# Kernel tuning notes

Hardware: AMD Instinct MI355X
Metric: run time of the kernel (lower is better)

## Reference

```python
import jax, jax.numpy as jnp
import numpy as np

B, D = 8192, 512
MARGIN, CR_BETA, NUM_CLASSES = 0.2, 0.1, 1000


def setup_inputs() -> dict:
    key = jax.random.key(0)
    k1, k2, k3, k4 = jax.random.split(key, 4)
    return {
        "img": jax.random.normal(k1, (B, D), jnp.float32),
        "txt": jax.random.normal(k2, (B, D), jnp.float32),
        "txt_cr": jax.random.normal(k3, (B, D), jnp.float32),
        "labels": jax.random.randint(k4, (B,), 0, NUM_CLASSES),
        "auto_margin_flag": 1,
        "margin": jnp.full((B,), MARGIN, jnp.float32),  # opt.margin repeated per row
        "cr_beta": CR_BETA,
    }


def _similarity(a, b):
    # row-normalize then full cosine-similarity matrix + matched (diagonal) sims
    an = a / (jnp.linalg.norm(a, axis=1, keepdims=True) + 1e-8)
    bn = b / (jnp.linalg.norm(b, axis=1, keepdims=True) + 1e-8)
    return an @ bn.T, jnp.sum(an * bn, axis=1)


def _dir_loss(sim, labels, margin, auto_flag):
    # semi-hard negative mining per anchor row, fully vectorized.
    # Deterministic stand-in for np.random.choice: first valid negative index.
    diag = jnp.diagonal(sim)                               # sim[idx, idx]
    neg_mask = labels[None, :] != labels[:, None]          # [B,B] negatives
    loss_mat = sim - diag[:, None] + margin[:, None]       # triplet margin term
    valid = neg_mask & (loss_mat > 0) & (loss_mat < margin[:, None])
    valid = jax.lax.stop_gradient(valid)                   # mining is detached (numpy in torch)
    has_valid = jnp.any(valid, axis=1)
    if auto_flag:
        row_ok = (margin >= 0.16) & has_valid
    else:
        row_ok = has_valid
    neg_idx = jnp.argmax(valid, axis=1)                    # first valid negative
    sim_an = jnp.take_along_axis(sim, neg_idx[:, None], axis=1)[:, 0]
    per_row = jax.nn.relu(margin - diag + sim_an)
    return jnp.sum(jnp.where(row_ok, per_row, 0.0))


def _cr_loss(img, txt, txt_cr, labels, auto_flag, margin, cr_beta):
    sim, sm = _similarity(img, txt)
    sim_cr, sm_cr = _similarity(img, txt_cr)
    if auto_flag:
        lam = jnp.abs(jax.lax.stop_gradient(sm_cr)) / jnp.abs(jax.lax.stop_gradient(sm))
        lam = jnp.minimum(lam, 1.0)                        # clamp lambda_cr to <= 1
        margin_cr = (lam + 1.0) * margin / 2.0
    else:
        margin_cr = margin / 2.0
    margin_cr = jax.lax.stop_gradient(margin_cr)
    base = _dir_loss(sim, labels, margin, auto_flag) + _dir_loss(sim.T, labels, margin, auto_flag)
    cr = _dir_loss(sim_cr, labels, margin_cr, auto_flag) + _dir_loss(sim_cr.T, labels, margin_cr, auto_flag)
    return base + cr_beta * cr


def reference(img, txt, txt_cr, labels, auto_margin_flag, margin, cr_beta):
    return _cr_loss(img, txt, txt_cr, labels, bool(auto_margin_flag), margin, cr_beta)
```

## Files before the change

kernel.cpp:

```cpp
#include <hip/hip_runtime.h>
#include <climits>

#define NB 8192
#define ND 512
#define NSPLIT 32
#define RSTART 64
#define RSPAN ((NB - RSTART + NSPLIT - 1) / NSPLIT)


__global__ __launch_bounds__(256) void stats_k(
        const float* __restrict__ img, const float* __restrict__ txt,
        const float* __restrict__ cr, const float* __restrict__ margin,
        const int* __restrict__ flagp,
        float* rnImg, float* rnTxt, float* rnCr,
        float* dgSim, float* dgCr, float* mgCr,
        int* negIdx, int* stragCnt, float* out) {
    int tid = threadIdx.x, bid = blockIdx.x;
    int g = bid * 256 + tid;
    if (g < 4 * NB) negIdx[g] = INT_MAX;
    if (bid == 0 && tid < 8) stragCnt[tid] = 0;
    if (bid == 0 && tid == 0) out[0] = 0.0f;

    int r = bid * 16 + (tid >> 4);
    int q = tid & 15;
    const float4* iv = (const float4*)(img + (size_t)r * ND);
    const float4* tv = (const float4*)(txt + (size_t)r * ND);
    const float4* cv = (const float4*)(cr  + (size_t)r * ND);
    float sii = 0, stt = 0, scc = 0, sit = 0, sic = 0;
    #pragma unroll
    for (int i = 0; i < 8; ++i) {
        int k = q + i * 16;
        float4 x = iv[k], y = tv[k], w = cv[k];
        sii += x.x*x.x + x.y*x.y + x.z*x.z + x.w*x.w;
        stt += y.x*y.x + y.y*y.y + y.z*y.z + y.w*y.w;
        scc += w.x*w.x + w.y*w.y + w.z*w.z + w.w*w.w;
        sit += x.x*y.x + x.y*y.y + x.z*y.z + x.w*y.w;
        sic += x.x*w.x + x.y*w.y + x.z*w.z + x.w*w.w;
    }
    #pragma unroll
    for (int off = 1; off < 16; off <<= 1) {
        sii += __shfl_xor(sii, off); stt += __shfl_xor(stt, off);
        scc += __shfl_xor(scc, off); sit += __shfl_xor(sit, off);
        sic += __shfl_xor(sic, off);
    }
    if (q == 0) {
        float rnI = 1.0f / (sqrtf(sii) + 1e-8f);
        float rnT = 1.0f / (sqrtf(stt) + 1e-8f);
        float rnC = 1.0f / (sqrtf(scc) + 1e-8f);
        float ds = sit * rnI * rnT;
        float dc = sic * rnI * rnC;
        float m  = margin[r];
        float mcr = flagp[0] ? (fminf(fabsf(dc) / fabsf(ds), 1.0f) + 1.0f) * m * 0.5f
                             : m * 0.5f;
        rnImg[r] = rnI; rnTxt[r] = rnT; rnCr[r] = rnC;
        dgSim[r] = ds;  dgCr[r]  = dc;  mgCr[r] = mcr;
    }
}

__device__ inline void pass_arrays(int z,
        const float* img, const float* txt, const float* cr,
        const float* rnImg, const float* rnTxt, const float* rnCr,
        const float* dgSim, const float* dgCr,
        const float* margin, const float* mgCr,
        const float*& A, const float*& B, const float*& rnA, const float*& rnB,
        const float*& dgA, const float*& mgA) {
    if (z == 0)      { A = img; B = txt; rnA = rnImg; rnB = rnTxt; dgA = dgSim; mgA = margin; }
    else if (z == 1) { A = txt; B = img; rnA = rnTxt; rnB = rnImg; dgA = dgSim; mgA = margin; }
    else if (z == 2) { A = img; B = cr;  rnA = rnImg; rnB = rnCr;  dgA = dgCr;  mgA = mgCr;   }
    else             { A = cr;  B = img; rnA = rnCr;  rnB = rnImg; dgA = dgCr;  mgA = mgCr;   }
}

__global__ __launch_bounds__(256) void band_k(
        const float* __restrict__ img, const float* __restrict__ txt,
        const float* __restrict__ cr, const int* __restrict__ labels,
        const int* __restrict__ flagp, const float* __restrict__ margin,
        const float* __restrict__ betap,
        const float* rnImg, const float* rnTxt, const float* rnCr,
        const float* dgSim, const float* dgCr, const float* mgCr,
        int* stragCnt, int* stragList, float* out) {
    __shared__ __align__(16) float As[16][64];
    __shared__ __align__(16) float Bs[16][64];
    __shared__ float aRn[64], aDg[64], aMg[64], colRn[64];
    __shared__ int   aLab[64], colLab[64], resIdx[64];
    __shared__ float blockAcc;

    const int tid = threadIdx.x, z = blockIdx.y, a0 = blockIdx.x * 64;
    const int flag = flagp[0];
    const float *A, *B, *rnA, *rnB, *dgA, *mgA;
    pass_arrays(z, img, txt, cr, rnImg, rnTxt, rnCr, dgSim, dgCr, margin, mgCr,
                A, B, rnA, rnB, dgA, mgA);

    if (tid < 64) {
        int a = a0 + tid;
        float mg = mgA[a];
        aRn[tid] = rnA[a]; aDg[tid] = dgA[a]; aMg[tid] = mg;
        aLab[tid] = labels[a];
        colRn[tid] = rnB[tid]; colLab[tid] = labels[tid];
        resIdx[tid] = (flag && mg < 0.16f) ? -1 : INT_MAX;
    }
    if (tid == 0) blockAcc = 0.0f;

    const int ty4  = (tid >> 4) * 4, tx4 = (tid & 15) * 4;
    const int lrow = tid >> 2,  lk4 = (tid & 3) * 4;

    float acc[4][4];
    #pragma unroll
    for (int i = 0; i < 4; ++i)
        #pragma unroll
        for (int j = 0; j < 4; ++j) acc[i][j] = 0.0f;

    float4 va = *(const float4*)(A + (size_t)(a0 + lrow) * ND + lk4);
    float4 vb = *(const float4*)(B + (size_t)lrow * ND + lk4);
    for (int kc = 0; kc < ND; kc += 16) {
        __syncthreads();
        As[lk4 + 0][lrow] = va.x; As[lk4 + 1][lrow] = va.y;
        As[lk4 + 2][lrow] = va.z; As[lk4 + 3][lrow] = va.w;
        Bs[lk4 + 0][lrow] = vb.x; Bs[lk4 + 1][lrow] = vb.y;
        Bs[lk4 + 2][lrow] = vb.z; Bs[lk4 + 3][lrow] = vb.w;
        if (kc + 16 < ND) {
            va = *(const float4*)(A + (size_t)(a0 + lrow) * ND + kc + 16 + lk4);
            vb = *(const float4*)(B + (size_t)lrow * ND + kc + 16 + lk4);
        }
        __syncthreads();
        #pragma unroll
        for (int k = 0; k < 16; ++k) {
            float4 av = *(const float4*)&As[k][ty4];
            float4 bv = *(const float4*)&Bs[k][tx4];
            float ar[4] = {av.x, av.y, av.z, av.w};
            float br[4] = {bv.x, bv.y, bv.z, bv.w};
            #pragma unroll
            for (int i = 0; i < 4; ++i)
                #pragma unroll
                for (int j = 0; j < 4; ++j)
                    acc[i][j] = fmaf(ar[i], br[j], acc[i][j]);
        }
    }
    __syncthreads();

    #pragma unroll
    for (int i = 0; i < 4; ++i) {
        int r = ty4 + i;
        float mgv = aMg[r];
        if (flag && mgv < 0.16f) continue;
        float dg = aDg[r], rna = aRn[r];
        int la = aLab[r];
        #pragma unroll
        for (int j = 0; j < 4; ++j) {
            int c = tx4 + j;
            if (colLab[c] == la) continue;
            float v  = acc[i][j] * rna * colRn[c];
            float lm = v - dg + mgv;
            if (lm > 0.0f && lm < mgv) atomicMin(&resIdx[r], c);
        }
    }
    __syncthreads();

    #pragma unroll
    for (int i = 0; i < 4; ++i) {
        int r = ty4 + i;
        int w = resIdx[r];
        if (w < 0 || w == INT_MAX) continue;
        int c = w - tx4;
        if (c < 0 || c > 3) continue;
        float v  = acc[i][c] * aRn[r] * colRn[w];
        float lm = v - aDg[r] + aMg[r];
        atomicAdd(&blockAcc, lm);
    }
    __syncthreads();

    if (tid < 64 && resIdx[tid] == INT_MAX) {
        int pos = atomicAdd(&stragCnt[z], 1);
        stragList[z * NB + pos] = a0 + tid;
    }
    if (tid == 0 && blockAcc != 0.0f) {
        float scale = (z >= 2) ? betap[0] : 1.0f;
        atomicAdd(out, blockAcc * scale);
    }
}

__device__ inline float dot8(const float4& a0, const float4& a1,
                             const float4& b0, const float4& b1) {
    return a0.x*b0.x + a0.y*b0.y + a0.z*b0.z + a0.w*b0.w
         + a1.x*b1.x + a1.y*b1.y + a1.z*b1.z + a1.w*b1.w;
}

__global__ __launch_bounds__(256) void strag_k(
        const float* __restrict__ img, const float* __restrict__ txt,
        const float* __restrict__ cr, const int* __restrict__ labels,
        const float* rnImg, const float* rnTxt, const float* rnCr,
        const float* dgSim, const float* dgCr,
        const float* __restrict__ margin, const float* mgCr,
        const int* stragCnt, const int* stragList, int* negIdx) {
    __shared__ float colDot[64];
    __shared__ int   cMin;
    __shared__ int   sharedG;
    const int tid = threadIdx.x;
    const int wv = tid >> 6, lane = tid & 63;

    const int s0c = stragCnt[0], s1c = stragCnt[1];
    const int s2c = stragCnt[2], s3c = stragCnt[3];
    const int ST = s0c + s1c + s2c + s3c;
    const int total = ST * NSPLIT;

    for (int it = blockIdx.x; it < total; it += gridDim.x) {
        int rg = it / ST;
        int sIdx = it - rg * ST;
        int z, s;
        if (sIdx < s0c)                 { z = 0; s = sIdx; }
        else if ((sIdx -= s0c) < s1c)   { z = 1; s = sIdx; }
        else if ((sIdx -= s1c) < s2c)   { z = 2; s = sIdx; }
        else                            { z = 3; s = sIdx - s2c; }
        const float *A, *B, *rnA, *rnB, *dgA, *mgA;
        pass_arrays(z, img, txt, cr, rnImg, rnTxt, rnCr, dgSim, dgCr,
                    margin, mgCr, A, B, rnA, rnB, dgA, mgA);
        int a = stragList[z * NB + s];
        int* gp = &negIdx[z * NB + a];
        const int start = RSTART + rg * RSPAN;
        const int rEnd = min(start + RSPAN, NB);

        __syncthreads();
        if (tid == 0) { cMin = INT_MAX; sharedG = atomicMin(gp, INT_MAX); }
        __syncthreads();
        int end = min(rEnd, sharedG);
        if (start >= end) continue;

        float rna = rnA[a], dgv = dgA[a], mgv = mgA[a];
        int la = labels[a];
        const float4* Av = (const float4*)(A + (size_t)a * ND);
        float4 ar0 = Av[lane], ar1 = Av[lane + 64];

        for (int j0 = start; j0 < end; j0 += 64) {
            #pragma unroll
            for (int g = 0; g < 2; ++g) {
                int cbase = j0 + wv * 16 + g * 8;
                float4 b0[8], b1[8];
                #pragma unroll
                for (int q = 0; q < 8; ++q) {
                    int col = cbase + q;
                    const float4* Bv = (col < end)
                        ? (const float4*)(B + (size_t)col * ND)
                        : (const float4*)B;
                    b0[q] = Bv[lane]; b1[q] = Bv[lane + 64];
                }
                float d[8];
                #pragma unroll
                for (int q = 0; q < 8; ++q) d[q] = dot8(ar0, ar1, b0[q], b1[q]);
                #pragma unroll
                for (int off = 1; off < 64; off <<= 1) {
                    #pragma unroll
                    for (int q = 0; q < 8; ++q) d[q] += __shfl_xor(d[q], off);
                }
                if (lane == 0) {
                    #pragma unroll
                    for (int q = 0; q < 8; ++q)
                        colDot[wv * 16 + g * 8 + q] = d[q];
                }
            }
            __syncthreads();
            if (tid < 64) {
                int col = j0 + tid;
                if (col < end && labels[col] != la) {
                    float lm = colDot[tid] * rna * rnB[col] - dgv + mgv;
                    if (lm > 0.0f && lm < mgv) atomicMin(&cMin, col);
                }
            } else if (tid == 64) {
                sharedG = atomicMin(gp, INT_MAX);
            }
            __syncthreads();
            int found = cMin;
            int gmin  = sharedG;
            if (found != INT_MAX) {
                if (tid == 0) atomicMin(gp, found);
                break;
            }
            if (gmin <= start) break;
            if (gmin < end) end = gmin;
        }
    }
}

__global__ __launch_bounds__(256) void final_k(
        const float* __restrict__ img, const float* __restrict__ txt,
        const float* __restrict__ cr,
        const float* rnImg, const float* rnTxt, const float* rnCr,
        const float* dgSim, const float* dgCr,
        const float* __restrict__ margin, const float* mgCr,
        const float* __restrict__ betap,
        const int* stragCnt, const int* stragList, const int* negIdx,
        float* out) {
    __shared__ float s4[4];
    const int tid = threadIdx.x, z = blockIdx.y;
    const float *A, *B, *rnA, *rnB, *dgA, *mgA;
    pass_arrays(z, img, txt, cr, rnImg, rnTxt, rnCr, dgSim, dgCr, margin, mgCr,
                A, B, rnA, rnB, dgA, mgA);
    int t = blockIdx.x * 256 + tid;
    float contrib = 0.0f;
    if (t < stragCnt[z]) {
        int a = stragList[z * NB + t];
        int idx = negIdx[z * NB + a];
        if (idx != INT_MAX) {
            const float4* Av = (const float4*)(A + (size_t)a   * ND);
            const float4* Bv = (const float4*)(B + (size_t)idx * ND);
            float d = 0.0f;
            #pragma unroll 8
            for (int i = 0; i < ND / 4; ++i) {
                float4 x = Av[i], y = Bv[i];
                d += x.x*y.x + x.y*y.y + x.z*y.z + x.w*y.w;
            }
            float lm = d * rnA[a] * rnB[idx] - dgA[a] + mgA[a];
            contrib = fmaxf(lm, 0.0f);
        }
    }
    #pragma unroll
    for (int off = 32; off; off >>= 1) contrib += __shfl_xor(contrib, off);
    if ((tid & 63) == 0) s4[tid >> 6] = contrib;
    __syncthreads();
    if (tid == 0) {
        float sum = s4[0] + s4[1] + s4[2] + s4[3];
        if (sum != 0.0f) atomicAdd(out, sum * ((z >= 2) ? betap[0] : 1.0f));
    }
}


__global__ __launch_bounds__(256) void zero_k(float* out, int n) {
    int g = blockIdx.x * 256 + threadIdx.x;
    if (g < n) out[g] = 0.0f;
}

template <int U>
__device__ void stragScan(const float* __restrict__ A, const float* __restrict__ B,
                          const int* __restrict__ labels, int a0, int u, int scol,
                          const int* sList, int g0,
                          const float* aRn, const float* aDg, const float* aMg,
                          const int* aLab, int* sMin8, int* doneMask,
                          float* blockAcc) {
    const int tid = threadIdx.x;
    float rn_s[U], dg_s[U], mg_s[U];
    int lab_s[U];
    const float4* Av[U];
    #pragma unroll
    for (int s = 0; s < U; ++s) {
        int slot = sList[g0 + (s < u ? s : 0)];
        rn_s[s] = aRn[slot]; dg_s[s] = aDg[slot]; mg_s[s] = aMg[slot];
        lab_s[s] = aLab[slot];
        Av[s] = (const float4*)(A + (size_t)(a0 + slot) * ND);
    }
    if (tid < U) sMin8[tid] = INT_MAX;
    if (tid == 0) *doneMask = 0;
    __syncthreads();
    for (int jb = scol; jb < NB; jb += 256) {
        int j = jb + tid;
        bool jv = (j < NB);
        int mask = *doneMask;
        float dot[U];
        #pragma unroll
        for (int s = 0; s < U; ++s) dot[s] = 0.0f;
        float ssq = 0.0f;
        if (jv) {
            const float4* Bv = (const float4*)(B + (size_t)j * ND);
            #pragma unroll 4
            for (int k4 = 0; k4 < ND / 4; ++k4) {
                float4 b = Bv[k4];
                ssq += b.x*b.x + b.y*b.y + b.z*b.z + b.w*b.w;
                #pragma unroll
                for (int s = 0; s < U; ++s) {
                    float4 a = Av[s][k4];
                    dot[s] += a.x*b.x + a.y*b.y + a.z*b.z + a.w*b.w;
                }
            }
        }
        float rnb = 1.0f / (sqrtf(ssq) + 1e-8f);
        int lj = jv ? labels[j] : -1;
        float lmv[U];
        #pragma unroll
        for (int s = 0; s < U; ++s) {
            lmv[s] = dot[s] * rn_s[s] * rnb - dg_s[s] + mg_s[s];
            if (jv && s < u && !((mask >> s) & 1) && lj != lab_s[s] &&
                lmv[s] > 0.0f && lmv[s] < mg_s[s])
                atomicMin(&sMin8[s], j);
        }
        __syncthreads();
        #pragma unroll
        for (int s = 0; s < U; ++s)
            if (jv && s < u && !((mask >> s) & 1) && sMin8[s] == j)
                atomicAdd(blockAcc, lmv[s]);
        __syncthreads();
        if (tid == 0) {
            int m2 = 0;
            for (int s = 0; s < u; ++s)
                if (sMin8[s] != INT_MAX) m2 |= (1 << s);
            *doneMask = m2;
        }
        __syncthreads();
        if (*doneMask == (1 << u) - 1) break;
    }
}

__global__ __launch_bounds__(256) void mine_k(const float* __restrict__ img,
                                              const float* __restrict__ txt,
                                              const float* __restrict__ cr,
                                              const int*   __restrict__ labels,
                                              const int*   __restrict__ flagp,
                                              const float* __restrict__ margin,
                                              const float* __restrict__ betap,
                                              float* __restrict__ out) {
    __shared__ __align__(16) float As[16][64];
    __shared__ __align__(16) float Bs[16][64];
    __shared__ float aRn[64], aDg[64], aMg[64];
    __shared__ int   aLab[64];
    __shared__ float colRn[64];
    __shared__ int   colLab[64];
    __shared__ int   resIdx[64], prevIdx[64];
    __shared__ int   cnt;
    __shared__ float blockAcc;
    __shared__ int   sList[64];
    __shared__ int   sCnt;
    __shared__ int   sMin8[8];
    __shared__ int   doneMask;

    const int tid  = threadIdx.x;
    const int z    = blockIdx.y;
    const int a0   = blockIdx.x * 64;
    const int flag = flagp[0];
    const float* A = (z == 1) ? txt : (z == 3) ? cr : img;
    const float* B = (z == 0) ? txt : (z == 2) ? cr : img;
    {
        int ar = tid >> 2, q = tid & 3;
        int a  = a0 + ar;
        const float4* iv = (const float4*)(img + (size_t)a * ND) + q * 32;
        const float4* tv = (const float4*)(txt + (size_t)a * ND) + q * 32;
        const float4* cv = (const float4*)(cr  + (size_t)a * ND) + q * 32;
        float sii = 0, stt = 0, scc = 0, sit = 0, sic = 0;
        #pragma unroll 4
        for (int i = 0; i < 32; ++i) {
            float4 x = iv[i], y = tv[i], w = cv[i];
            sii += x.x*x.x + x.y*x.y + x.z*x.z + x.w*x.w;
            stt += y.x*y.x + y.y*y.y + y.z*y.z + y.w*y.w;
            scc += w.x*w.x + w.y*w.y + w.z*w.z + w.w*w.w;
            sit += x.x*y.x + x.y*y.y + x.z*y.z + x.w*y.w;
            sic += x.x*w.x + x.y*w.y + x.z*w.z + x.w*w.w;
        }
        sii += __shfl_xor(sii, 1); sii += __shfl_xor(sii, 2);
        stt += __shfl_xor(stt, 1); stt += __shfl_xor(stt, 2);
        sit += __shfl_xor(sit, 1); sit += __shfl_xor(sit, 2);
        scc += __shfl_xor(scc, 1); scc += __shfl_xor(scc, 2);
        sic += __shfl_xor(sic, 1); sic += __shfl_xor(sic, 2);
        if (q == 0) {
            float rnI = 1.0f / (sqrtf(sii) + 1e-8f);
            float rnT = 1.0f / (sqrtf(stt) + 1e-8f);
            float ds  = sit * rnI * rnT;
            float m   = margin[a];
            float mg, rna, dgv;
            if (z >= 2) {
                float rnC = 1.0f / (sqrtf(scc) + 1e-8f);
                float dc  = sic * rnI * rnC;
                mg = flag ? (fminf(fabsf(dc) / fabsf(ds), 1.0f) + 1.0f) * m * 0.5f
                          : m * 0.5f;
                dgv = dc; rna = (z == 3) ? rnC : rnI;
            } else {
                mg = m; dgv = ds; rna = (z == 1) ? rnT : rnI;
            }
            aRn[ar] = rna; aDg[ar] = dgv; aMg[ar] = mg; aLab[ar] = labels[a];
            resIdx[ar] = (flag && mg < 0.16f) ? -1 : INT_MAX;
        }
        if (tid == 0) blockAcc = 0.0f;
    }
    __syncthreads();
    const int ty4  = (tid >> 4) * 4, tx4 = (tid & 15) * 4;
    const int lrow = tid >> 2,  lk4 = (tid & 3) * 4;
    int bandCols = 0, unresolved = 64;
    for (int jc = 0; jc < 2; ++jc) {
        int j0 = jc * 64;
        float acc[4][4];
        #pragma unroll
        for (int i = 0; i < 4; ++i)
            #pragma unroll
            for (int j = 0; j < 4; ++j) acc[i][j] = 0.0f;
        float bssq = 0.0f;
        for (int kc = 0; kc < ND; kc += 16) {
            __syncthreads();
            float4 va = *(const float4*)(A + (size_t)(a0 + lrow) * ND + kc + lk4);
            float4 vb = *(const float4*)(B + (size_t)(j0 + lrow) * ND + kc + lk4);
            As[lk4 + 0][lrow] = va.x; As[lk4 + 1][lrow] = va.y;
            As[lk4 + 2][lrow] = va.z; As[lk4 + 3][lrow] = va.w;
            Bs[lk4 + 0][lrow] = vb.x; Bs[lk4 + 1][lrow] = vb.y;
            Bs[lk4 + 2][lrow] = vb.z; Bs[lk4 + 3][lrow] = vb.w;
            bssq += vb.x*vb.x + vb.y*vb.y + vb.z*vb.z + vb.w*vb.w;
            __syncthreads();
            #pragma unroll
            for (int k = 0; k < 16; ++k) {
                float4 av = *(const float4*)&As[k][ty4];
                float4 bv = *(const float4*)&Bs[k][tx4];
                float ar[4] = {av.x, av.y, av.z, av.w};
                float br[4] = {bv.x, bv.y, bv.z, bv.w};
                #pragma unroll
                for (int i = 0; i < 4; ++i)
                    #pragma unroll
                    for (int j = 0; j < 4; ++j)
                        acc[i][j] = fmaf(ar[i], br[j], acc[i][j]);
            }
        }
        bssq += __shfl_xor(bssq, 1); bssq += __shfl_xor(bssq, 2);
        __syncthreads();
        if ((tid & 3) == 0) {
            colRn[lrow]  = 1.0f / (sqrtf(bssq) + 1e-8f);
            colLab[lrow] = labels[j0 + lrow];
        }
        if (tid < 64) prevIdx[tid] = resIdx[tid];
        __syncthreads();
        #pragma unroll
        for (int i = 0; i < 4; ++i) {
            int r = ty4 + i;
            if (prevIdx[r] != INT_MAX) continue;
            float dg = aDg[r], mgv = aMg[r], rna = aRn[r];
            int la = aLab[r];
            #pragma unroll
            for (int j = 0; j < 4; ++j) {
                int c = tx4 + j;
                if (colLab[c] == la) continue;
                float v  = acc[i][j] * rna * colRn[c];
                float lm = v - dg + mgv;
                if (lm > 0.0f && lm < mgv) atomicMin(&resIdx[r], j0 + c);
            }
        }
        __syncthreads();
        #pragma unroll
        for (int i = 0; i < 4; ++i) {
            int r = ty4 + i;
            if (prevIdx[r] != INT_MAX) continue;
            int w = resIdx[r];
            if (w == INT_MAX) continue;
            int c = w - j0 - tx4;
            if (c < 0 || c > 3) continue;
            float v  = acc[i][c] * aRn[r] * colRn[tx4 + c];
            float lm = v - aDg[r] + aMg[r];
            atomicAdd(&blockAcc, lm);
        }
        __syncthreads();
        if (tid == 0) cnt = 0;
        __syncthreads();
        if (tid < 64 && resIdx[tid] == INT_MAX) atomicAdd(&cnt, 1);
        __syncthreads();
        unresolved = cnt;
        bandCols = j0 + 64;
        __syncthreads();
        if (unresolved <= 8) break;
    }
    if (unresolved > 0) {
        if (tid == 0) sCnt = 0;
        __syncthreads();
        if (tid < 64 && resIdx[tid] == INT_MAX) {
            int pos = atomicAdd(&sCnt, 1);
            sList[pos] = tid;
        }
        __syncthreads();
        int total = sCnt;
        for (int g0 = 0; g0 < total; g0 += 8) {
            int u = min(8, total - g0);
            if (u == 1)      stragScan<1>(A, B, labels, a0, u, bandCols, sList, g0, aRn, aDg, aMg, aLab, sMin8, &doneMask, &blockAcc);
            else if (u == 2) stragScan<2>(A, B, labels, a0, u, bandCols, sList, g0, aRn, aDg, aMg, aLab, sMin8, &doneMask, &blockAcc);
            else if (u <= 4) stragScan<4>(A, B, labels, a0, u, bandCols, sList, g0, aRn, aDg, aMg, aLab, sMin8, &doneMask, &blockAcc);
            else             stragScan<8>(A, B, labels, a0, u, bandCols, sList, g0, aRn, aDg, aMg, aLab, sMin8, &doneMask, &blockAcc);
            __syncthreads();
        }
    }
    if (tid == 0 && blockAcc != 0.0f) {
        float scale = (z >= 2) ? betap[0] : 1.0f;
        atomicAdd(out, blockAcc * scale);
    }
}


extern "C" void kernel_launch(void* const* d_in, const int* in_sizes, int n_in,
                              void* d_out, int out_size, void* d_ws, size_t ws_size,
                              hipStream_t stream) {
    const float* img    = (const float*)d_in[0];
    const float* txt    = (const float*)d_in[1];
    const float* cr     = (const float*)d_in[2];
    const int*   labels = (const int*)  d_in[3];
    const int*   flagp  = (const int*)  d_in[4];
    const float* marg   = (const float*)d_in[5];
    const float* betap  = (const float*)d_in[6];
    float* out = (float*)d_out;
    (void)in_sizes; (void)n_in;

    const size_t REQ = (size_t)(6 * NB) * 4 + (size_t)(4 * NB) * 4 + 64 +
                       (size_t)(4 * NB) * 4;
    if (ws_size >= REQ) {
        float* wf = (float*)d_ws;
        float* rnImg = wf + 0 * NB;
        float* rnTxt = wf + 1 * NB;
        float* rnCr  = wf + 2 * NB;
        float* dgSim = wf + 3 * NB;
        float* dgCr  = wf + 4 * NB;
        float* mgCr  = wf + 5 * NB;
        int* negIdx    = (int*)(wf + 6 * NB);
        int* stragCnt  = negIdx + 4 * NB;
        int* stragList = stragCnt + 16;

        stats_k<<<dim3(NB / 16),      dim3(256), 0, stream>>>(
            img, txt, cr, marg, flagp,
            rnImg, rnTxt, rnCr, dgSim, dgCr, mgCr, negIdx, stragCnt, out);
        band_k <<<dim3(NB / 64, 4),   dim3(256), 0, stream>>>(
            img, txt, cr, labels, flagp, marg, betap,
            rnImg, rnTxt, rnCr, dgSim, dgCr, mgCr, stragCnt, stragList, out);
        strag_k<<<dim3(16384),        dim3(256), 0, stream>>>(
            img, txt, cr, labels, rnImg, rnTxt, rnCr, dgSim, dgCr, marg, mgCr,
            stragCnt, stragList, negIdx);
        final_k<<<dim3(NB / 256, 4),  dim3(256), 0, stream>>>(
            img, txt, cr, rnImg, rnTxt, rnCr, dgSim, dgCr, marg, mgCr, betap,
            stragCnt, stragList, negIdx, out);
    } else {
        zero_k<<<dim3((out_size + 255) / 256), dim3(256), 0, stream>>>(out, out_size);
        mine_k<<<dim3(NB / 64, 4), dim3(256), 0, stream>>>(img, txt, cr, labels,
                                                           flagp, marg, betap, out);
    }
}
```

Measured before the change: 221.6 us.

## Split straggler search into short sequential scan and split-range hard pass

Straggler rows are now first scanned sequentially over a short window of columns by one block each, with early exit once a valid negative is found. Rows still unresolved are appended to a hard list, which a second kernel searches over the remaining columns split into 31 ranges, as before. The aim is to stop launching 32 range-blocks per straggler when most find a negative early. It adds a kernel launch, an extra atomic-counted list and more workspace.

```diff
diff --git a/kernel.cpp b/kernel.cpp
--- a/kernel.cpp
+++ b/kernel.cpp
@@ -3,9 +3,11 @@
 
 #define NB 8192
 #define ND 512
-#define NSPLIT 32
 #define RSTART 64
-#define RSPAN ((NB - RSTART + NSPLIT - 1) / NSPLIT)
+#define RSPAN_A 256
+#define NSPLIT_B 31
+#define BSTART (RSTART + RSPAN_A)
+#define RSPAN_B (((NB - BSTART) + NSPLIT_B - 1) / NSPLIT_B)
 
 
 __global__ __launch_bounds__(256) void stats_k(
@@ -14,11 +16,12 @@
         const int* __restrict__ flagp,
         float* rnImg, float* rnTxt, float* rnCr,
         float* dgSim, float* dgCr, float* mgCr,
-        int* negIdx, int* stragCnt, float* out) {
+        int* negIdx, int* stragCnt, int* hardCnt, float* out) {
     int tid = threadIdx.x, bid = blockIdx.x;
     int g = bid * 256 + tid;
     if (g < 4 * NB) negIdx[g] = INT_MAX;
     if (bid == 0 && tid < 8) stragCnt[tid] = 0;
+    if (bid == 0 && tid >= 8 && tid < 16) hardCnt[tid - 8] = 0;
     if (bid == 0 && tid == 0) out[0] = 0.0f;
 
     int r = bid * 16 + (tid >> 4);
@@ -184,27 +187,25 @@
          + a1.x*b1.x + a1.y*b1.y + a1.z*b1.z + a1.w*b1.w;
 }
 
-__global__ __launch_bounds__(256) void strag_k(
+__global__ __launch_bounds__(256) void strag_a_k(
         const float* __restrict__ img, const float* __restrict__ txt,
         const float* __restrict__ cr, const int* __restrict__ labels,
         const float* rnImg, const float* rnTxt, const float* rnCr,
         const float* dgSim, const float* dgCr,
         const float* __restrict__ margin, const float* mgCr,
-        const int* stragCnt, const int* stragList, int* negIdx) {
+        const int* stragCnt, const int* stragList, int* negIdx,
+        int* hardCnt, int* hardList) {
     __shared__ float colDot[64];
     __shared__ int   cMin;
-    __shared__ int   sharedG;
     const int tid = threadIdx.x;
     const int wv = tid >> 6, lane = tid & 63;
 
     const int s0c = stragCnt[0], s1c = stragCnt[1];
     const int s2c = stragCnt[2], s3c = stragCnt[3];
     const int ST = s0c + s1c + s2c + s3c;
-    const int total = ST * NSPLIT;
-
-    for (int it = blockIdx.x; it < total; it += gridDim.x) {
-        int rg = it / ST;
-        int sIdx = it - rg * ST;
+
+    for (int it = blockIdx.x; it < ST; it += gridDim.x) {
+        int sIdx = it;
         int z, s;
         if (sIdx < s0c)                 { z = 0; s = sIdx; }
         else if ((sIdx -= s0c) < s1c)   { z = 1; s = sIdx; }
@@ -214,9 +215,92 @@
         pass_arrays(z, img, txt, cr, rnImg, rnTxt, rnCr, dgSim, dgCr,
                     margin, mgCr, A, B, rnA, rnB, dgA, mgA);
         int a = stragList[z * NB + s];
-        int* gp = &negIdx[z * NB + a];
-        const int start = RSTART + rg * RSPAN;
-        const int rEnd = min(start + RSPAN, NB);
+
+        __syncthreads();
+        if (tid == 0) cMin = INT_MAX;
+        __syncthreads();
+
+        float rna = rnA[a], dgv = dgA[a], mgv = mgA[a];
+        int la = labels[a];
+        const float4* Av = (const float4*)(A + (size_t)a * ND);
+        float4 ar0 = Av[lane], ar1 = Av[lane + 64];
+        const int endA = RSTART + RSPAN_A;
+
+        for (int j0 = RSTART; j0 < endA; j0 += 64) {
+            #pragma unroll
+            for (int g = 0; g < 2; ++g) {
+                int cbase = j0 + wv * 16 + g * 8;
+                float4 b0[8], b1[8];
+                #pragma unroll
+                for (int q = 0; q < 8; ++q) {
+                    int col = cbase + q;
+                    const float4* Bv = (col < endA)
+                        ? (const float4*)(B + (size_t)col * ND)
+                        : (const float4*)B;
+                    b0[q] = Bv[lane]; b1[q] = Bv[lane + 64];
+                }
+                float d[8];
+                #pragma unroll
+                for (int q = 0; q < 8; ++q) d[q] = dot8(ar0, ar1, b0[q], b1[q]);
+                #pragma unroll
+                for (int off = 1; off < 64; off <<= 1) {
+                    #pragma unroll
+                    for (int q = 0; q < 8; ++q) d[q] += __shfl_xor(d[q], off);
+                }
+                if (lane == 0) {
+                    #pragma unroll
+                    for (int q = 0; q < 8; ++q)
+                        colDot[wv * 16 + g * 8 + q] = d[q];
+                }
+            }
+            __syncthreads();
+            if (tid < 64) {
+                int col = j0 + tid;
+                if (col < endA && labels[col] != la) {
+                    float lm = colDot[tid] * rna * rnB[col] - dgv + mgv;
+                    if (lm > 0.0f && lm < mgv) atomicMin(&cMin, col);
+                }
+            }
+            __syncthreads();
+            if (cMin != INT_MAX) break;
+        }
+        if (tid == 0) {
+            if (cMin != INT_MAX) negIdx[z * NB + a] = cMin;
+            else {
+                int p = atomicAdd(hardCnt, 1);
+                hardList[p] = z * NB + a;
+            }
+        }
+    }
+}
+
+__global__ __launch_bounds__(256) void strag_b_k(
+        const float* __restrict__ img, const float* __restrict__ txt,
+        const float* __restrict__ cr, const int* __restrict__ labels,
+        const float* rnImg, const float* rnTxt, const float* rnCr,
+        const float* dgSim, const float* dgCr,
+        const float* __restrict__ margin, const float* mgCr,
+        const int* hardCnt, const int* hardList, int* negIdx) {
+    __shared__ float colDot[64];
+    __shared__ int   cMin;
+    __shared__ int   sharedG;
+    const int tid = threadIdx.x;
+    const int wv = tid >> 6, lane = tid & 63;
+
+    const int hc = hardCnt[0];
+    const int total = hc * NSPLIT_B;
+
+    for (int it = blockIdx.x; it < total; it += gridDim.x) {
+        int rg = it / hc;
+        int h  = it - rg * hc;
+        int za = hardList[h];
+        int z = za >> 13, a = za & (NB - 1);
+        const float *A, *B, *rnA, *rnB, *dgA, *mgA;
+        pass_arrays(z, img, txt, cr, rnImg, rnTxt, rnCr, dgSim, dgCr,
+                    margin, mgCr, A, B, rnA, rnB, dgA, mgA);
+        int* gp = &negIdx[za];
+        const int start = BSTART + rg * RSPAN_B;
+        const int rEnd = min(start + RSPAN_B, NB);
 
         __syncthreads();
         if (tid == 0) { cMin = INT_MAX; sharedG = atomicMin(gp, INT_MAX); }
@@ -584,8 +668,12 @@
     float* out = (float*)d_out;
     (void)in_sizes; (void)n_in;
 
-    const size_t REQ = (size_t)(6 * NB) * 4 + (size_t)(4 * NB) * 4 + 64 +
-                       (size_t)(4 * NB) * 4;
+    const size_t REQ = (size_t)(6 * NB) * 4
+                     + (size_t)(4 * NB) * 4
+                     + 64
+                     + (size_t)(4 * NB) * 4
+                     + 64
+                     + (size_t)(4 * NB) * 4;
     if (ws_size >= REQ) {
         float* wf = (float*)d_ws;
         float* rnImg = wf + 0 * NB;
@@ -597,17 +685,22 @@
         int* negIdx    = (int*)(wf + 6 * NB);
         int* stragCnt  = negIdx + 4 * NB;
         int* stragList = stragCnt + 16;
-
-        stats_k<<<dim3(NB / 16),      dim3(256), 0, stream>>>(
+        int* hardCnt   = stragList + 4 * NB;
+        int* hardList  = hardCnt + 16;
+
+        stats_k <<<dim3(NB / 16),     dim3(256), 0, stream>>>(
             img, txt, cr, marg, flagp,
-            rnImg, rnTxt, rnCr, dgSim, dgCr, mgCr, negIdx, stragCnt, out);
-        band_k <<<dim3(NB / 64, 4),   dim3(256), 0, stream>>>(
+            rnImg, rnTxt, rnCr, dgSim, dgCr, mgCr, negIdx, stragCnt, hardCnt, out);
+        band_k  <<<dim3(NB / 64, 4),  dim3(256), 0, stream>>>(
             img, txt, cr, labels, flagp, marg, betap,
             rnImg, rnTxt, rnCr, dgSim, dgCr, mgCr, stragCnt, stragList, out);
-        strag_k<<<dim3(16384),        dim3(256), 0, stream>>>(
+        strag_a_k<<<dim3(2048),       dim3(256), 0, stream>>>(
             img, txt, cr, labels, rnImg, rnTxt, rnCr, dgSim, dgCr, marg, mgCr,
-            stragCnt, stragList, negIdx);
-        final_k<<<dim3(NB / 256, 4),  dim3(256), 0, stream>>>(
+            stragCnt, stragList, negIdx, hardCnt, hardList);
+        strag_b_k<<<dim3(8192),       dim3(256), 0, stream>>>(
+            img, txt, cr, labels, rnImg, rnTxt, rnCr, dgSim, dgCr, marg, mgCr,
+            hardCnt, hardList, negIdx);
+        final_k <<<dim3(NB / 256, 4), dim3(256), 0, stream>>>(
             img, txt, cr, rnImg, rnTxt, rnCr, dgSim, dgCr, marg, mgCr, betap,
             stragCnt, stragList, negIdx, out);
     } else {
```

Result: no change. 224.4 us (+1.3%).
